# Kernel optimization log

Hardware: AMD Instinct MI355X
Metric: run time of the kernel (lower is better)

Reference implementation:

```python
import jax, jax.numpy as jnp
import numpy as np

N, D, F_NUM = 262144, 128, 64
TEMPERATURE = 0.5
EPS = 1e-8  # torch F.cosine_similarity eps


def setup_inputs() -> dict:
    key = jax.random.key(0)
    k1, k2 = jax.random.split(key)
    embeddings = jax.random.normal(k1, (N, D), dtype=jnp.float32)
    families = jax.random.randint(k2, (N,), 0, F_NUM, dtype=jnp.int32)
    return {"embeddings": embeddings, "families": families}


def reference(embeddings, families):
    T = TEMPERATURE
    n = embeddings.shape[0]
    # Per-family prototype means (segment mean). All F_NUM families are
    # present w.h.p.; guard counts with max(.,1) to avoid div-by-zero.
    ones = jnp.ones((n,), dtype=embeddings.dtype)
    counts = jax.ops.segment_sum(ones, families, num_segments=F_NUM)
    sums = jax.ops.segment_sum(embeddings, families, num_segments=F_NUM)
    protos = sums / jnp.maximum(counts, 1.0)[:, None]  # [F, D]

    # Cosine similarity matrix [N, F], matching torch eps semantics:
    # x.y / max(||x|| * ||y||, eps)
    dots = embeddings @ protos.T                              # [N, F]
    e_norm = jnp.linalg.norm(embeddings, axis=1)              # [N]
    p_norm = jnp.linalg.norm(protos, axis=1)                  # [F]
    sim = dots / jnp.maximum(e_norm[:, None] * p_norm[None, :], EPS)

    pos = jnp.take_along_axis(sim, families[:, None].astype(jnp.int32), axis=1)[:, 0]  # [N]
    # Source quirk: logits already divided by T, then divided by T again
    # inside logsumexp -> effective sim / T^2. The concatenated logits
    # contain pos + all other prototypes = all F prototypes exactly once.
    lse = jax.nn.logsumexp(sim / (T * T), axis=1)             # [N]
    per_sample = -pos / T + lse                               # [N]
    loss = jnp.sum(per_sample) / n
    return loss[None]  # torch returns shape (1,)
```

## Files before the change

### kernel.cpp

```cpp
#include <hip/hip_runtime.h>
#include <math.h>


#define D_DIM 128
#define F_NUM 64

typedef __attribute__((ext_vector_type(8))) short short8;
typedef __attribute__((ext_vector_type(4))) float f32x4;

static __device__ __forceinline__ unsigned short f2bf(float x) {
  union { float f; unsigned u; } v; v.f = x;
  unsigned r = v.u + 0x7FFFu + ((v.u >> 16) & 1u);
  return (unsigned short)(r >> 16);
}

__global__ __launch_bounds__(256) void pass_a(
    const float* __restrict__ emb, const int* __restrict__ fam,
    float* __restrict__ psum, unsigned int* __restrict__ ehat)
{
  __shared__ float acc[4 * F_NUM * D_DIM];
  int t = threadIdx.x;
  float4 z = make_float4(0.f, 0.f, 0.f, 0.f);
  float4* a4 = (float4*)acc;
  #pragma unroll
  for (int k = 0; k < 32; ++k) a4[t + k * 256] = z;
  __syncthreads();

  int w = t >> 6, l = t & 63;
  float* my = acc + w * 8192;
  int base = __builtin_amdgcn_readfirstlane(blockIdx.x * 1024 + w * 256);
  const float2* e2 = (const float2*)emb;

  #pragma unroll 1
  for (int b = 0; b < 16; ++b) {
    float2 v[16]; int f[16];
    #pragma unroll
    for (int j = 0; j < 16; ++j) {
      int r = base + b * 16 + j;
      v[j] = e2[(size_t)r * 64 + l];
      f[j] = fam[r];
    }
    #pragma unroll
    for (int j = 0; j < 16; ++j) {
      float x = v[j].x, y = v[j].y;
      float nq = x * x + y * y;
      nq += __shfl_xor(nq, 1);  nq += __shfl_xor(nq, 2);  nq += __shfl_xor(nq, 4);
      nq += __shfl_xor(nq, 8);  nq += __shfl_xor(nq, 16); nq += __shfl_xor(nq, 32);
      float inv = rsqrtf(fmaxf(nq, 1e-20f));
      ehat[(size_t)(base + b * 16 + j) * 64 + l] =
          ((unsigned)f2bf(y * inv) << 16) | f2bf(x * inv);
      float2* dst = (float2*)&my[f[j] * D_DIM + 2 * l];
      float2 cur = *dst;
      cur.x += x; cur.y += y;
      *dst = cur;
    }
  }
  __syncthreads();

  float4* out4 = (float4*)(psum + (size_t)blockIdx.x * (F_NUM * D_DIM));
  #pragma unroll
  for (int k = 0; k < 8; ++k) {
    int idx4 = t + k * 256;
    float4 r = z;
    #pragma unroll
    for (int rp = 0; rp < 4; ++rp) {
      float4 a = a4[rp * 2048 + idx4];
      r.x += a.x; r.y += a.y; r.z += a.z; r.w += a.w;
    }
    out4[idx4] = r;
  }
}

__global__ __launch_bounds__(256) void pass_b1(
    const float* __restrict__ psum, float* __restrict__ protoRaw, int nPart)
{
  __shared__ float red[256];
  int f = blockIdx.x >> 2, qd = blockIdx.x & 3;
  int t = threadIdx.x;
  int d = qd * 32 + (t & 31), p0 = t >> 5;
  int per = nPart >> 3;
  float s = 0.f;
  #pragma unroll 8
  for (int i = 0; i < per; ++i)
    s += psum[(size_t)(p0 + 8 * i) * (F_NUM * D_DIM) + f * D_DIM + d];
  red[t] = s;
  __syncthreads();
  if (t < 32) {
    float r = 0.f;
    #pragma unroll
    for (int k = 0; k < 8; ++k) r += red[k * 32 + t];
    protoRaw[f * D_DIM + qd * 32 + t] = r;
  }
}

__global__ __launch_bounds__(256) void pass_b2(
    const float* __restrict__ protoRaw, unsigned short* __restrict__ protoB)
{
  int t = threadIdx.x, f = t >> 2, pt = t & 3;
  const float4* src = (const float4*)(protoRaw + f * D_DIM + pt * 32);
  float4 v[8];
  float n2 = 0.f;
  #pragma unroll
  for (int i = 0; i < 8; ++i) {
    v[i] = src[i];
    n2 += v[i].x * v[i].x + v[i].y * v[i].y + v[i].z * v[i].z + v[i].w * v[i].w;
  }
  n2 += __shfl_xor(n2, 1);
  n2 += __shfl_xor(n2, 2);
  float inv = rsqrtf(fmaxf(n2, 1e-24f));
  ushort4* dst = (ushort4*)(protoB + f * D_DIM + pt * 32);
  #pragma unroll
  for (int i = 0; i < 8; ++i) {
    ushort4 u;
    u.x = f2bf(v[i].x * inv); u.y = f2bf(v[i].y * inv);
    u.z = f2bf(v[i].z * inv); u.w = f2bf(v[i].w * inv);
    dst[i] = u;
  }
}

__global__ __launch_bounds__(256) void pass_c(
    const unsigned short* __restrict__ ehat, const int* __restrict__ fam,
    const unsigned short* __restrict__ protoB,
    float* __restrict__ out, float invN)
{
  __shared__ __align__(16) unsigned short sA[128 * 136];
  __shared__ __align__(16) unsigned short sB[F_NUM * 136];
  __shared__ int   sFam[128];
  __shared__ float sWp[4];

  int t = threadIdx.x;
  int R0 = blockIdx.x * 128;
  const short8* srcA = (const short8*)ehat;
  const short8* srcB = (const short8*)protoB;

  #pragma unroll
  for (int it = 0; it < 8; ++it) {
    int idx = it * 256 + t;
    int row = idx >> 4, c8 = idx & 15;
    *(short8*)&sA[row * 136 + c8 * 8] = srcA[(size_t)(R0 + row) * 16 + c8];
  }
  #pragma unroll
  for (int it = 0; it < 4; ++it) {
    int idx = it * 256 + t;
    int row = idx >> 4, c8 = idx & 15;
    *(short8*)&sB[row * 136 + c8 * 8] = srcB[idx];
  }
  if (t < 128) sFam[t] = fam[R0 + t];
  __syncthreads();

  int w = t >> 6, lane = t & 63, m16 = lane & 15, q = lane >> 4;

  f32x4 acc[2][4] = {};
  const unsigned short* aB0 = &sA[(w * 32 + m16) * 136 + q * 8];
  const unsigned short* aB1 = aB0 + 16 * 136;
  const unsigned short* bB  = &sB[m16 * 136 + q * 8];

  #pragma unroll
  for (int ks = 0; ks < 4; ++ks) {
    int ko = ks * 32;
    short8 a0 = *(const short8*)(aB0 + ko);
    short8 a1 = *(const short8*)(aB1 + ko);
    short8 b0 = *(const short8*)(bB + ko);
    short8 b1 = *(const short8*)(bB + 16 * 136 + ko);
    short8 b2 = *(const short8*)(bB + 32 * 136 + ko);
    short8 b3 = *(const short8*)(bB + 48 * 136 + ko);
    acc[0][0] = __builtin_amdgcn_mfma_f32_16x16x32_bf16(a0, b0, acc[0][0], 0, 0, 0);
    acc[0][1] = __builtin_amdgcn_mfma_f32_16x16x32_bf16(a0, b1, acc[0][1], 0, 0, 0);
    acc[0][2] = __builtin_amdgcn_mfma_f32_16x16x32_bf16(a0, b2, acc[0][2], 0, 0, 0);
    acc[0][3] = __builtin_amdgcn_mfma_f32_16x16x32_bf16(a0, b3, acc[0][3], 0, 0, 0);
    acc[1][0] = __builtin_amdgcn_mfma_f32_16x16x32_bf16(a1, b0, acc[1][0], 0, 0, 0);
    acc[1][1] = __builtin_amdgcn_mfma_f32_16x16x32_bf16(a1, b1, acc[1][1], 0, 0, 0);
    acc[1][2] = __builtin_amdgcn_mfma_f32_16x16x32_bf16(a1, b2, acc[1][2], 0, 0, 0);
    acc[1][3] = __builtin_amdgcn_mfma_f32_16x16x32_bf16(a1, b3, acc[1][3], 0, 0, 0);
  }

  float wp = 0.f;
  #pragma unroll
  for (int rt = 0; rt < 2; ++rt) {
    #pragma unroll
    for (int i = 0; i < 4; ++i) {
      int row = w * 32 + rt * 16 + q * 4 + i;
      int fr = sFam[row], frh = fr >> 4, frl = fr & 15;
      float es = 0.f, ps = 0.f;
      #pragma unroll
      for (int ft = 0; ft < 4; ++ft) {
        float sim = acc[rt][ft][i];
        es += __expf(4.f * sim - 4.f);
        if (frl == m16 && frh == ft) ps = sim;
      }
      #pragma unroll
      for (int off = 1; off < 16; off <<= 1) {
        es += __shfl_xor(es, off);
        ps += __shfl_xor(ps, off);
      }
      if (m16 == 0) wp += 4.f + __logf(es) - 2.f * ps;
    }
  }
  wp += __shfl_xor(wp, 16);
  wp += __shfl_xor(wp, 32);
  if (lane == 0) sWp[w] = wp;
  __syncthreads();
  if (t == 0)
    unsafeAtomicAdd(out, (sWp[0] + sWp[1] + sWp[2] + sWp[3]) * invN);
}

extern "C" void kernel_launch(void* const* d_in, const int* in_sizes, int n_in,
                              void* d_out, int out_size, void* d_ws, size_t ws_size,
                              hipStream_t stream) {
  const float* emb = (const float*)d_in[0];
  const int* fam = (const int*)d_in[1];
  int N = in_sizes[0] / D_DIM;
  int blocksA = N / 1024;
  int blocksC = N / 128;

  float* ws = (float*)d_ws;
  float* psum = ws;
  size_t off = (size_t)blocksA * (F_NUM * D_DIM);
  float* protoRaw = ws + off;                off += F_NUM * D_DIM;
  unsigned short* protoB = (unsigned short*)(ws + off); off += (F_NUM * D_DIM) / 2;
  unsigned int* ehat = (unsigned int*)(ws + off);

  (void)hipMemsetAsync(d_out, 0, sizeof(float), stream);
  pass_a<<<blocksA, 256, 0, stream>>>(emb, fam, psum, ehat);
  pass_b1<<<4 * F_NUM, 256, 0, stream>>>(psum, protoRaw, blocksA);
  pass_b2<<<1, 256, 0, stream>>>(protoRaw, protoB);
  pass_c<<<blocksC, 256, 0, stream>>>((const unsigned short*)ehat, fam, protoB,
                                      (float*)d_out, 1.0f / (float)N);
}
```

Before: 248.2 us.

## Recompute normalized bf16 embeddings in pass_c instead of storing ehat; merge duplicate-family adds

Pass A no longer writes a normalized bf16 copy of the embeddings. Pass C instead rereads the fp32 embeddings, converts them to bf16 unnormalized, and applies the inverse row norm after the MFMA. This removes a write and a read of the 64MB bf16 intermediate but doubles pass C's input reads. Pass A also merges same-family rows within groups of four in registers, using a dummy row 65 as a sink, to cut LDS read-modify-write traffic. An inert leftover loop remains in pass C.

```diff
diff --git a/kernel.cpp b/kernel.cpp
--- a/kernel.cpp
+++ b/kernel.cpp
@@ -4,6 +4,8 @@
 
 #define D_DIM 128
 #define F_NUM 64
+#define AROWS 65
+#define AST (AROWS * D_DIM)
 
 typedef __attribute__((ext_vector_type(8))) short short8;
 typedef __attribute__((ext_vector_type(4))) float f32x4;
@@ -16,18 +18,17 @@
 
 __global__ __launch_bounds__(256) void pass_a(
     const float* __restrict__ emb, const int* __restrict__ fam,
-    float* __restrict__ psum, unsigned int* __restrict__ ehat)
-{
-  __shared__ float acc[4 * F_NUM * D_DIM];
+    float* __restrict__ psum)
+{
+  __shared__ float acc[4 * AST];
   int t = threadIdx.x;
   float4 z = make_float4(0.f, 0.f, 0.f, 0.f);
   float4* a4 = (float4*)acc;
-  #pragma unroll
-  for (int k = 0; k < 32; ++k) a4[t + k * 256] = z;
+  for (int i = t; i < AST; i += 256) a4[i] = z;
   __syncthreads();
 
   int w = t >> 6, l = t & 63;
-  float* my = acc + w * 8192;
+  float* my = acc + w * AST;
   int base = __builtin_amdgcn_readfirstlane(blockIdx.x * 1024 + w * 256);
   const float2* e2 = (const float2*)emb;
 
@@ -41,18 +42,30 @@
       f[j] = fam[r];
     }
     #pragma unroll
-    for (int j = 0; j < 16; ++j) {
-      float x = v[j].x, y = v[j].y;
-      float nq = x * x + y * y;
-      nq += __shfl_xor(nq, 1);  nq += __shfl_xor(nq, 2);  nq += __shfl_xor(nq, 4);
-      nq += __shfl_xor(nq, 8);  nq += __shfl_xor(nq, 16); nq += __shfl_xor(nq, 32);
-      float inv = rsqrtf(fmaxf(nq, 1e-20f));
-      ehat[(size_t)(base + b * 16 + j) * 64 + l] =
-          ((unsigned)f2bf(y * inv) << 16) | f2bf(x * inv);
-      float2* dst = (float2*)&my[f[j] * D_DIM + 2 * l];
-      float2 cur = *dst;
-      cur.x += x; cur.y += y;
-      *dst = cur;
+    for (int s4 = 0; s4 < 4; ++s4) {
+      int jj = s4 * 4;
+      #pragma unroll
+      for (int k = 1; k < 4; ++k) {
+        #pragma unroll
+        for (int j = 0; j < k; ++j) {
+          if (f[jj + j] == f[jj + k]) {
+            v[jj + j].x += v[jj + k].x;
+            v[jj + j].y += v[jj + k].y;
+            f[jj + k] = 64;
+          }
+        }
+      }
+      float2 cur[4];
+      #pragma unroll
+      for (int j = 0; j < 4; ++j)
+        cur[j] = *(float2*)&my[f[jj + j] * D_DIM + 2 * l];
+      #pragma unroll
+      for (int j = 0; j < 4; ++j) {
+        cur[j].x += v[jj + j].x; cur[j].y += v[jj + j].y;
+      }
+      #pragma unroll
+      for (int j = 0; j < 4; ++j)
+        *(float2*)&my[f[jj + j] * D_DIM + 2 * l] = cur[j];
     }
   }
   __syncthreads();
@@ -61,10 +74,11 @@
   #pragma unroll
   for (int k = 0; k < 8; ++k) {
     int idx4 = t + k * 256;
+    int ff = idx4 >> 5, c4 = idx4 & 31;
     float4 r = z;
     #pragma unroll
     for (int rp = 0; rp < 4; ++rp) {
-      float4 a = a4[rp * 2048 + idx4];
+      float4 a = *(const float4*)&acc[rp * AST + ff * D_DIM + c4 * 4];
       r.x += a.x; r.y += a.y; r.z += a.z; r.w += a.w;
     }
     out4[idx4] = r;
@@ -119,31 +133,45 @@
 }
 
 __global__ __launch_bounds__(256) void pass_c(
-    const unsigned short* __restrict__ ehat, const int* __restrict__ fam,
+    const float* __restrict__ emb, const int* __restrict__ fam,
     const unsigned short* __restrict__ protoB,
     float* __restrict__ out, float invN)
 {
   __shared__ __align__(16) unsigned short sA[128 * 136];
   __shared__ __align__(16) unsigned short sB[F_NUM * 136];
+  __shared__ float sInvE[128];
   __shared__ int   sFam[128];
   __shared__ float sWp[4];
 
   int t = threadIdx.x;
   int R0 = blockIdx.x * 128;
-  const short8* srcA = (const short8*)ehat;
-  const short8* srcB = (const short8*)protoB;
-
+  const float4* src = (const float4*)emb;
+
+  #pragma unroll
+  for (int it = 0; it < 16; ++it) {
+    int idx = it * 256 + t;
+    int row = idx >> 5, c4 = idx & 31;
+    float4 v = src[(size_t)(R0 + row) * 32 + c4];
+    float nq = v.x * v.x + v.y * v.y + v.z * v.z + v.w * v.w;
+    nq += __shfl_xor(nq, 1);  nq += __shfl_xor(nq, 2);  nq += __shfl_xor(nq, 4);
+    nq += __shfl_xor(nq, 8);  nq += __shfl_xor(nq, 16);
+    if ((t & 31) == 0) sInvE[row] = rsqrtf(fmaxf(nq, 1e-20f));
+    ushort4 u;
+    u.x = f2bf(v.x); u.y = f2bf(v.y); u.z = f2bf(v.z); u.w = f2bf(v.w);
+    *(ushort4*)&sA[row * 136 + (c4 << 2)] = u;
+  }
+  const ushort4* pb = (const ushort4*)protoB;
+  #pragma unroll
+  for (int it = 0; it < 4; ++it) {
+    int idx = it * 256 + t;
+    int f = idx >> 4, c4 = idx & 15;
+    (void)f; (void)c4;
+  }
   #pragma unroll
   for (int it = 0; it < 8; ++it) {
     int idx = it * 256 + t;
-    int row = idx >> 4, c8 = idx & 15;
-    *(short8*)&sA[row * 136 + c8 * 8] = srcA[(size_t)(R0 + row) * 16 + c8];
-  }
-  #pragma unroll
-  for (int it = 0; it < 4; ++it) {
-    int idx = it * 256 + t;
-    int row = idx >> 4, c8 = idx & 15;
-    *(short8*)&sB[row * 136 + c8 * 8] = srcB[idx];
+    int f = idx >> 5, c4 = idx & 31;
+    *(ushort4*)&sB[f * 136 + (c4 << 2)] = pb[idx];
   }
   if (t < 128) sFam[t] = fam[R0 + t];
   __syncthreads();
@@ -180,11 +208,12 @@
     #pragma unroll
     for (int i = 0; i < 4; ++i) {
       int row = w * 32 + rt * 16 + q * 4 + i;
+      float inv_e = sInvE[row];
       int fr = sFam[row], frh = fr >> 4, frl = fr & 15;
       float es = 0.f, ps = 0.f;
       #pragma unroll
       for (int ft = 0; ft < 4; ++ft) {
-        float sim = acc[rt][ft][i];
+        float sim = acc[rt][ft][i] * inv_e;
         es += __expf(4.f * sim - 4.f);
         if (frl == m16 && frh == ft) ps = sim;
       }
@@ -217,13 +246,12 @@
   float* psum = ws;
   size_t off = (size_t)blocksA * (F_NUM * D_DIM);
   float* protoRaw = ws + off;                off += F_NUM * D_DIM;
-  unsigned short* protoB = (unsigned short*)(ws + off); off += (F_NUM * D_DIM) / 2;
-  unsigned int* ehat = (unsigned int*)(ws + off);
+  unsigned short* protoB = (unsigned short*)(ws + off);
 
   (void)hipMemsetAsync(d_out, 0, sizeof(float), stream);
-  pass_a<<<blocksA, 256, 0, stream>>>(emb, fam, psum, ehat);
+  pass_a<<<blocksA, 256, 0, stream>>>(emb, fam, psum);
   pass_b1<<<4 * F_NUM, 256, 0, stream>>>(psum, protoRaw, blocksA);
   pass_b2<<<1, 256, 0, stream>>>(protoRaw, protoB);
-  pass_c<<<blocksC, 256, 0, stream>>>((const unsigned short*)ehat, fam, protoB,
+  pass_c<<<blocksC, 256, 0, stream>>>(emb, fam, protoB,
                                       (float*)d_out, 1.0f / (float)N);
 }
```

Result: no change. 252.3 us (+1.6%).

## Prefetch next batch, dedupe scatter conflicts, fuse prototype reduce+normalize, trim shuffles

Applied to the files above, without the earlier changes.

In pass_a, the next batch of 16 rows is loaded from global memory into registers before the current batch is processed. Scatter-adds into shared memory are now done in groups of 4, with rows of the same family pre-summed and the duplicates sent to a dummy row 65, so the loads and stores within a group can be issued independently. pass_b1 and pass_b2 are merged into one kernel with 64 blocks, which drops a launch and the protoRaw round trip but gives less parallelism in the psum reduction. In pass_c, the positive-similarity shuffle reduction is moved out of the per-row loop into a single final reduction.

```diff
diff --git a/kernel.cpp b/kernel.cpp
--- a/kernel.cpp
+++ b/kernel.cpp
@@ -4,6 +4,8 @@
 
 #define D_DIM 128
 #define F_NUM 64
+#define AROWS 65
+#define AST (AROWS * D_DIM)
 
 typedef __attribute__((ext_vector_type(8))) short short8;
 typedef __attribute__((ext_vector_type(4))) float f32x4;
@@ -18,28 +20,37 @@
     const float* __restrict__ emb, const int* __restrict__ fam,
     float* __restrict__ psum, unsigned int* __restrict__ ehat)
 {
-  __shared__ float acc[4 * F_NUM * D_DIM];
+  __shared__ float acc[4 * AST];
   int t = threadIdx.x;
   float4 z = make_float4(0.f, 0.f, 0.f, 0.f);
   float4* a4 = (float4*)acc;
-  #pragma unroll
-  for (int k = 0; k < 32; ++k) a4[t + k * 256] = z;
+  for (int i = t; i < AST; i += 256) a4[i] = z;
   __syncthreads();
 
   int w = t >> 6, l = t & 63;
-  float* my = acc + w * 8192;
+  float* my = acc + w * AST;
   int base = __builtin_amdgcn_readfirstlane(blockIdx.x * 1024 + w * 256);
   const float2* e2 = (const float2*)emb;
 
+  float2 v[16]; int f[16];
+  #pragma unroll
+  for (int j = 0; j < 16; ++j) {
+    v[j] = e2[(size_t)(base + j) * 64 + l];
+    f[j] = fam[base + j];
+  }
+
   #pragma unroll 1
   for (int b = 0; b < 16; ++b) {
-    float2 v[16]; int f[16];
-    #pragma unroll
-    for (int j = 0; j < 16; ++j) {
-      int r = base + b * 16 + j;
-      v[j] = e2[(size_t)r * 64 + l];
-      f[j] = fam[r];
-    }
+    float2 vn[16]; int fn[16];
+    if (b < 15) {
+      int nb = base + (b + 1) * 16;
+      #pragma unroll
+      for (int j = 0; j < 16; ++j) {
+        vn[j] = e2[(size_t)(nb + j) * 64 + l];
+        fn[j] = fam[nb + j];
+      }
+    }
+
     #pragma unroll
     for (int j = 0; j < 16; ++j) {
       float x = v[j].x, y = v[j].y;
@@ -49,11 +60,37 @@
       float inv = rsqrtf(fmaxf(nq, 1e-20f));
       ehat[(size_t)(base + b * 16 + j) * 64 + l] =
           ((unsigned)f2bf(y * inv) << 16) | f2bf(x * inv);
-      float2* dst = (float2*)&my[f[j] * D_DIM + 2 * l];
-      float2 cur = *dst;
-      cur.x += x; cur.y += y;
-      *dst = cur;
-    }
+    }
+
+    #pragma unroll
+    for (int s4 = 0; s4 < 4; ++s4) {
+      int jj = s4 * 4;
+      #pragma unroll
+      for (int k = 1; k < 4; ++k) {
+        #pragma unroll
+        for (int j = 0; j < k; ++j) {
+          if (f[jj + j] == f[jj + k]) {
+            v[jj + j].x += v[jj + k].x;
+            v[jj + j].y += v[jj + k].y;
+            f[jj + k] = 64;
+          }
+        }
+      }
+      float2 cur[4];
+      #pragma unroll
+      for (int j = 0; j < 4; ++j)
+        cur[j] = *(float2*)&my[f[jj + j] * D_DIM + 2 * l];
+      #pragma unroll
+      for (int j = 0; j < 4; ++j) {
+        cur[j].x += v[jj + j].x; cur[j].y += v[jj + j].y;
+      }
+      #pragma unroll
+      for (int j = 0; j < 4; ++j)
+        *(float2*)&my[f[jj + j] * D_DIM + 2 * l] = cur[j];
+    }
+
+    #pragma unroll
+    for (int j = 0; j < 16; ++j) { v[j] = vn[j]; f[j] = fn[j]; }
   }
   __syncthreads();
 
@@ -61,60 +98,45 @@
   #pragma unroll
   for (int k = 0; k < 8; ++k) {
     int idx4 = t + k * 256;
+    int ff = idx4 >> 5, c4 = idx4 & 31;
     float4 r = z;
     #pragma unroll
     for (int rp = 0; rp < 4; ++rp) {
-      float4 a = a4[rp * 2048 + idx4];
+      float4 a = *(const float4*)&acc[rp * AST + ff * D_DIM + c4 * 4];
       r.x += a.x; r.y += a.y; r.z += a.z; r.w += a.w;
     }
     out4[idx4] = r;
   }
 }
 
-__global__ __launch_bounds__(256) void pass_b1(
-    const float* __restrict__ psum, float* __restrict__ protoRaw, int nPart)
+__global__ __launch_bounds__(256) void pass_b(
+    const float* __restrict__ psum, unsigned short* __restrict__ protoB,
+    int nPart)
 {
   __shared__ float red[256];
-  int f = blockIdx.x >> 2, qd = blockIdx.x & 3;
-  int t = threadIdx.x;
-  int d = qd * 32 + (t & 31), p0 = t >> 5;
-  int per = nPart >> 3;
+  __shared__ float prot[128];
+  __shared__ float nrm[2];
+  int fb = blockIdx.x, t = threadIdx.x;
+  int d = t & 127, h = t >> 7;
+  int per = nPart >> 1;
   float s = 0.f;
   #pragma unroll 8
   for (int i = 0; i < per; ++i)
-    s += psum[(size_t)(p0 + 8 * i) * (F_NUM * D_DIM) + f * D_DIM + d];
+    s += psum[(size_t)(h + 2 * i) * (F_NUM * D_DIM) + fb * D_DIM + d];
   red[t] = s;
   __syncthreads();
-  if (t < 32) {
-    float r = 0.f;
-    #pragma unroll
-    for (int k = 0; k < 8; ++k) r += red[k * 32 + t];
-    protoRaw[f * D_DIM + qd * 32 + t] = r;
-  }
-}
-
-__global__ __launch_bounds__(256) void pass_b2(
-    const float* __restrict__ protoRaw, unsigned short* __restrict__ protoB)
-{
-  int t = threadIdx.x, f = t >> 2, pt = t & 3;
-  const float4* src = (const float4*)(protoRaw + f * D_DIM + pt * 32);
-  float4 v[8];
-  float n2 = 0.f;
-  #pragma unroll
-  for (int i = 0; i < 8; ++i) {
-    v[i] = src[i];
-    n2 += v[i].x * v[i].x + v[i].y * v[i].y + v[i].z * v[i].z + v[i].w * v[i].w;
-  }
-  n2 += __shfl_xor(n2, 1);
-  n2 += __shfl_xor(n2, 2);
-  float inv = rsqrtf(fmaxf(n2, 1e-24f));
-  ushort4* dst = (ushort4*)(protoB + f * D_DIM + pt * 32);
-  #pragma unroll
-  for (int i = 0; i < 8; ++i) {
-    ushort4 u;
-    u.x = f2bf(v[i].x * inv); u.y = f2bf(v[i].y * inv);
-    u.z = f2bf(v[i].z * inv); u.w = f2bf(v[i].w * inv);
-    dst[i] = u;
+  if (t < 128) {
+    float p = red[t] + red[t + 128];
+    prot[t] = p;
+    float q = p * p;
+    q += __shfl_xor(q, 1);  q += __shfl_xor(q, 2);  q += __shfl_xor(q, 4);
+    q += __shfl_xor(q, 8);  q += __shfl_xor(q, 16); q += __shfl_xor(q, 32);
+    if ((t & 63) == 0) nrm[t >> 6] = q;
+  }
+  __syncthreads();
+  if (t < 128) {
+    float inv = rsqrtf(fmaxf(nrm[0] + nrm[1], 1e-24f));
+    protoB[fb * D_DIM + t] = f2bf(prot[t] * inv);
   }
 }
 
@@ -174,31 +196,32 @@
     acc[1][3] = __builtin_amdgcn_mfma_f32_16x16x32_bf16(a1, b3, acc[1][3], 0, 0, 0);
   }
 
-  float wp = 0.f;
+  float wp = 0.f, m2ps = 0.f;
   #pragma unroll
   for (int rt = 0; rt < 2; ++rt) {
     #pragma unroll
     for (int i = 0; i < 4; ++i) {
       int row = w * 32 + rt * 16 + q * 4 + i;
       int fr = sFam[row], frh = fr >> 4, frl = fr & 15;
-      float es = 0.f, ps = 0.f;
+      float es = 0.f;
       #pragma unroll
       for (int ft = 0; ft < 4; ++ft) {
         float sim = acc[rt][ft][i];
         es += __expf(4.f * sim - 4.f);
-        if (frl == m16 && frh == ft) ps = sim;
-      }
-      #pragma unroll
-      for (int off = 1; off < 16; off <<= 1) {
-        es += __shfl_xor(es, off);
-        ps += __shfl_xor(ps, off);
-      }
-      if (m16 == 0) wp += 4.f + __logf(es) - 2.f * ps;
-    }
-  }
-  wp += __shfl_xor(wp, 16);
-  wp += __shfl_xor(wp, 32);
-  if (lane == 0) sWp[w] = wp;
+        if (frl == m16 && frh == ft) m2ps += sim;
+      }
+      es += __shfl_xor(es, 1);
+      es += __shfl_xor(es, 2);
+      es += __shfl_xor(es, 4);
+      es += __shfl_xor(es, 8);
+      if (m16 == 0) wp += 4.f + __logf(es);
+    }
+  }
+  float tot = wp - 2.f * m2ps;
+  tot += __shfl_xor(tot, 1);  tot += __shfl_xor(tot, 2);
+  tot += __shfl_xor(tot, 4);  tot += __shfl_xor(tot, 8);
+  tot += __shfl_xor(tot, 16); tot += __shfl_xor(tot, 32);
+  if (lane == 0) sWp[w] = tot;
   __syncthreads();
   if (t == 0)
     unsafeAtomicAdd(out, (sWp[0] + sWp[1] + sWp[2] + sWp[3]) * invN);
@@ -216,14 +239,12 @@
   float* ws = (float*)d_ws;
   float* psum = ws;
   size_t off = (size_t)blocksA * (F_NUM * D_DIM);
-  float* protoRaw = ws + off;                off += F_NUM * D_DIM;
   unsigned short* protoB = (unsigned short*)(ws + off); off += (F_NUM * D_DIM) / 2;
   unsigned int* ehat = (unsigned int*)(ws + off);
 
   (void)hipMemsetAsync(d_out, 0, sizeof(float), stream);
   pass_a<<<blocksA, 256, 0, stream>>>(emb, fam, psum, ehat);
-  pass_b1<<<4 * F_NUM, 256, 0, stream>>>(psum, protoRaw, blocksA);
-  pass_b2<<<1, 256, 0, stream>>>(protoRaw, protoB);
+  pass_b<<<F_NUM, 256, 0, stream>>>(psum, protoB, blocksA);
   pass_c<<<blocksC, 256, 0, stream>>>((const unsigned short*)ehat, fam, protoB,
                                       (float*)d_out, 1.0f / (float)N);
 }
```

New measurement: 254.7 us. 2.6% more time.
